# Kernel tuning notes

Hardware: AMD Instinct MI355X
Metric: run time of the kernel (lower is better)

Reference implementation:

```python
import jax, jax.numpy as jnp
import numpy as np

D_MODEL = 1024
N_HEADS = 16
D_HEAD = D_MODEL // N_HEADS


def setup_inputs() -> dict:
    key = jax.random.key(0)
    ks = jax.random.split(key, 5)
    scale = 1.0 / np.sqrt(D_MODEL)
    x = jax.random.normal(ks[0], (4, 2048, D_MODEL), dtype=jnp.float32)
    w_qkv = jax.random.normal(ks[1], (D_MODEL, 3 * D_MODEL), dtype=jnp.float32) * scale
    b_qkv = jax.random.normal(ks[2], (3 * D_MODEL,), dtype=jnp.float32) * 0.02
    w_out = jax.random.normal(ks[3], (D_MODEL, D_MODEL), dtype=jnp.float32) * scale
    b_out = jax.random.normal(ks[4], (D_MODEL,), dtype=jnp.float32) * 0.02
    return {"x": x, "w_qkv": w_qkv, "b_qkv": b_qkv, "w_out": w_out, "b_out": b_out}


def reference(x, w_qkv, b_qkv, w_out, b_out):
    b, s, _ = x.shape
    qkv = jnp.einsum("bsd,de->bse", x, w_qkv) + b_qkv  # [b, s, 3*d_model]
    q, k, v = jnp.split(qkv, 3, axis=-1)
    # [b, s, d_model] -> [b, h, s, d_head]
    def heads(t):
        return t.reshape(b, s, N_HEADS, D_HEAD).transpose(0, 2, 1, 3)
    q, k, v = heads(q), heads(k), heads(v)
    scale = 1.0 / np.sqrt(D_HEAD).astype(np.float32)
    attn = jnp.einsum("bhqd,bhkd->bhqk", q, k) * scale  # [b, h, s, s]
    attn = jax.nn.softmax(attn, axis=-1)
    out = jnp.einsum("bhqk,bhkd->bhqd", attn, v)  # [b, h, s, d_head]
    out = out.transpose(0, 2, 1, 3).reshape(b, s, D_MODEL)
    return jnp.einsum("bsd,de->bse", out, w_out) + b_out
```

## Files before the change

### kernel.cpp

```cpp
#include <hip/hip_runtime.h>
#include <hip/hip_bf16.h>

typedef unsigned short u16;
typedef unsigned int u32;
typedef __attribute__((ext_vector_type(8))) short bf16x8;
typedef __attribute__((ext_vector_type(4))) float f32x4;
typedef __attribute__((ext_vector_type(16))) float f32x16;

#define MFMA16(a, b, c) __builtin_amdgcn_mfma_f32_16x16x32_bf16((a), (b), (c), 0, 0, 0)
#define MFMA32(a, b, c) __builtin_amdgcn_mfma_f32_32x32x16_bf16((a), (b), (c), 0, 0, 0)

__device__ __forceinline__ u16 f2bf(float f) {
    u32 u;
    __builtin_memcpy(&u, &f, 4);
    u32 r = (u + 0x7FFFu + ((u >> 16) & 1u)) >> 16;
    return (u16)r;
}

__device__ __forceinline__ u32 pk_bf16(float a, float b) {
    u32 r;
    asm("v_cvt_pk_bf16_f32 %0, %1, %2" : "=v"(r) : "v"(a), "v"(b));
    return r;
}

__device__ __forceinline__ void gload16(const void* g, void* l) {
    __builtin_amdgcn_global_load_lds((const __attribute__((address_space(1))) u32*)g,
                                     (__attribute__((address_space(3))) u32*)l, 16, 0, 0);
}

__global__ __launch_bounds__(256) void cvt_bf16(const float* __restrict__ in, u16* __restrict__ out) {
    size_t i = ((size_t)blockIdx.x * 256 + threadIdx.x) * 8;
    f32x4 a = *(const f32x4*)(in + i);
    f32x4 b = *(const f32x4*)(in + i + 4);
    union {
        bf16x8 v;
        u16 s[8];
    } r;
    r.s[0] = f2bf(a[0]);
    r.s[1] = f2bf(a[1]);
    r.s[2] = f2bf(a[2]);
    r.s[3] = f2bf(a[3]);
    r.s[4] = f2bf(b[0]);
    r.s[5] = f2bf(b[1]);
    r.s[6] = f2bf(b[2]);
    r.s[7] = f2bf(b[3]);
    *(bf16x8*)(out + i) = r.v;
}

__global__ __launch_bounds__(256) void transpose_f32_bf16(const float* __restrict__ in,
                                                          u16* __restrict__ out, int R, int C) {
    __shared__ u16 t[64][65];
    const int c0 = blockIdx.x * 64, r0 = blockIdx.y * 64;
    const int tid = threadIdx.x;
#pragma unroll
    for (int i = 0; i < 16; ++i) {
        int idx = i * 256 + tid;
        int r = idx >> 6, c = idx & 63;
        t[r][c] = f2bf(in[(size_t)(r0 + r) * C + c0 + c]);
    }
    __syncthreads();
#pragma unroll
    for (int i = 0; i < 16; ++i) {
        int idx = i * 256 + tid;
        int cc = idx >> 6, rr = idx & 63;
        out[(size_t)(c0 + cc) * R + r0 + rr] = t[rr][cc];
    }
}

template <int ROWS>
__device__ __forceinline__ void stage_tile(const u16* gbase, int stride_e, u16* lds, int tid) {
    const int wbase16 = (tid & ~63) * 8;
#pragma unroll
    for (int i = 0; i < ROWS / 32; ++i) {
        int chunk = i * 256 + tid;
        int r = chunk >> 3;
        int c = chunk & 7;
        int sc = c ^ (r & 7);
        const u16* src = gbase + (size_t)r * stride_e + sc * 8;
        u16* dst = lds + i * 2048 + wbase16;
        gload16(src, dst);
    }
}

#define QSCALE 0.1803368801111243f

__global__ __launch_bounds__(256) void gemm_bt(const u16* __restrict__ A, const u16* __restrict__ Bt,
                                               const float* __restrict__ bias, u16* __restrict__ Cb,
                                               u16* __restrict__ vt, float* __restrict__ Cf, int M,
                                               int N, int K, int Cstride, int split) {
    __shared__ __align__(16) u16 As[128 * 64];
    __shared__ __align__(16) u16 Bs[128 * 64];
    const int tid = threadIdx.x;
    const int lane = tid & 63, wid = tid >> 6;
    const int wr = wid >> 1, wc = wid & 1;
    const int g = lane >> 4, l15 = lane & 15;
    const int m0 = blockIdx.y * 128, n0 = blockIdx.x * 128;

    f32x4 acc[4][4] = {};

    for (int k0 = 0; k0 < K; k0 += 64) {
        __syncthreads();
        stage_tile<128>(A + (size_t)m0 * K + k0, K, As, tid);
        stage_tile<128>(Bt + (size_t)n0 * K + k0, K, Bs, tid);
        __syncthreads();
        bf16x8 af[4][2], bf[4][2];
#pragma unroll
        for (int m = 0; m < 4; ++m) {
            int row = wr * 64 + m * 16 + l15;
#pragma unroll
            for (int t = 0; t < 2; ++t) {
                int off = row * 128 + (((t * 4 + g) ^ (row & 7)) * 16);
                af[m][t] = *(const bf16x8*)((const char*)As + off);
            }
        }
#pragma unroll
        for (int n = 0; n < 4; ++n) {
            int row = wc * 64 + n * 16 + l15;
#pragma unroll
            for (int t = 0; t < 2; ++t) {
                int off = row * 128 + (((t * 4 + g) ^ (row & 7)) * 16);
                bf[n][t] = *(const bf16x8*)((const char*)Bs + off);
            }
        }
#pragma unroll
        for (int m = 0; m < 4; ++m)
#pragma unroll
            for (int n = 0; n < 4; ++n) {
                acc[m][n] = MFMA16(af[m][0], bf[n][0], acc[m][n]);
                acc[m][n] = MFMA16(af[m][1], bf[n][1], acc[m][n]);
            }
    }

#pragma unroll
    for (int m = 0; m < 4; ++m) {
        int row0 = m0 + wr * 64 + m * 16 + g * 4;
#pragma unroll
        for (int n = 0; n < 4; ++n) {
            int col = n0 + wc * 64 + n * 16 + l15;
            float bs = bias ? bias[col] : 0.0f;
            if (!split) {
#pragma unroll
                for (int rr = 0; rr < 4; ++rr)
                    Cf[(size_t)(row0 + rr) * Cstride + col] = acc[m][n][rr] + bs;
            } else {
                if (col < 2048) {
                    float scale = (col < 1024) ? QSCALE : 1.0f;
#pragma unroll
                    for (int rr = 0; rr < 4; ++rr)
                        Cb[(size_t)(row0 + rr) * 2048 + col] = f2bf((acc[m][n][rr] + bs) * scale);
                } else {
                    int e2 = col - 2048;
                    int h = e2 >> 6, dh = e2 & 63;
                    int b = row0 >> 11, s = row0 & 2047;
                    u32 lo = pk_bf16(acc[m][n][0] + bs, acc[m][n][1] + bs);
                    u32 hi = pk_bf16(acc[m][n][2] + bs, acc[m][n][3] + bs);
                    u32* dst = (u32*)&vt[((size_t)((b * 16 + h) * 64 + dh)) * 2048 + s];
                    dst[0] = lo;
                    dst[1] = hi;
                }
            }
        }
    }
}

__global__ __launch_bounds__(256, 4) void attn_fwd(const u16* __restrict__ qk,
                                                   const u16* __restrict__ vt,
                                                   u16* __restrict__ out) {
    __shared__ __align__(16) u16 Ks[2][64 * 64];
    __shared__ __align__(16) u16 Vs[2][64 * 64];
    const int tid = threadIdx.x;
    const int lane = tid & 63, w = tid >> 6;
    const int hi = lane >> 5, l31 = lane & 31;
    const int bh = blockIdx.y, b = bh >> 4, h = bh & 15;
    const int q0w = blockIdx.x * 128 + w * 32;
    const size_t qrowbase = (size_t)b * 2048 + q0w;

    bf16x8 qf[4];
#pragma unroll
    for (int c = 0; c < 4; ++c)
        qf[c] = *(const bf16x8*)&qk[(qrowbase + l31) * 2048 + h * 64 + c * 16 + hi * 8];

    float l_r = 0.f;
    f32x16 acc[2] = {};
    const f32x16 FZERO = {};

    const u16* kbase = qk + (size_t)b * 2048 * 2048 + 1024 + h * 64;
    const u16* vbase = vt + (size_t)bh * 64 * 2048;

    const int wb16 = (tid & ~63) * 8;
    const int ch0 = tid, ch1 = 256 + tid;
    const int r0c = ch0 >> 3, s0c = (ch0 & 7) ^ (r0c & 7);
    const int r1c = ch1 >> 3, s1c = (ch1 & 7) ^ (r1c & 7);
    const u16* kp0 = kbase + r0c * 2048 + s0c * 8;
    const u16* kp1 = kbase + r1c * 2048 + s1c * 8;
    const u16* vp0 = vbase + r0c * 2048 + s0c * 8;
    const u16* vp1 = vbase + r1c * 2048 + s1c * 8;
    const int KADV = 64 * 2048;

    const int swz8 = l31 & 7;
    const int rowB = l31 * 128;
    int exorH[4];
#pragma unroll
    for (int c = 0; c < 4; ++c) exorH[c] = ((2 * c + hi) ^ swz8) * 16;
    int exorV[2][2];
#pragma unroll
    for (int kb = 0; kb < 2; ++kb)
#pragma unroll
        for (int t = 0; t < 2; ++t) exorV[kb][t] = ((4 * kb + 2 * t + hi) ^ swz8) * 16;

    {
        u16* kd = &Ks[0][0] + wb16;
        u16* vd = &Vs[0][0] + wb16;
        gload16(kp0, kd);
        gload16(kp1, kd + 2048);
        gload16(vp0, vd);
        gload16(vp1, vd + 2048);
        kp0 += KADV;
        kp1 += KADV;
        vp0 += 64;
        vp1 += 64;
    }
    __syncthreads();

    int cur = 0;
    for (int kv0 = 0; kv0 < 2048; kv0 += 64) {
        if (kv0 + 64 < 2048) {
            u16* kd = &Ks[cur ^ 1][0] + wb16;
            u16* vd = &Vs[cur ^ 1][0] + wb16;
            gload16(kp0, kd);
            gload16(kp1, kd + 2048);
            gload16(vp0, vd);
            gload16(vp1, vd + 2048);
            kp0 += KADV;
            kp1 += KADV;
            vp0 += 64;
            vp1 += 64;
        }
        const char* ksr = (const char*)&Ks[cur][0] + rowB;
        const char* vsr = (const char*)&Vs[cur][0] + rowB;

        f32x16 sA, sB;
        {
            bf16x8 ka0 = *(const bf16x8*)(ksr + exorH[0]);
            bf16x8 kb0 = *(const bf16x8*)(ksr + exorH[0] + 4096);
            sA = MFMA32(ka0, qf[0], FZERO);
            sB = MFMA32(kb0, qf[0], FZERO);
#pragma unroll
            for (int c = 1; c < 4; ++c) {
                bf16x8 ka = *(const bf16x8*)(ksr + exorH[c]);
                bf16x8 kb = *(const bf16x8*)(ksr + exorH[c] + 4096);
                sA = MFMA32(ka, qf[c], sA);
                sB = MFMA32(kb, qf[c], sB);
            }
        }

#pragma unroll
        for (int kb = 0; kb < 2; ++kb) {
            const f32x16& s = kb ? sB : sA;
            float rs0 = 0.f, rs1 = 0.f;
            u32 pk[8];
#pragma unroll
            for (int j = 0; j < 8; ++j) {
                float p0 = __builtin_amdgcn_exp2f(s[2 * j]);
                float p1 = __builtin_amdgcn_exp2f(s[2 * j + 1]);
                rs0 += p0;
                rs1 += p1;
                pk[j] = pk_bf16(p0, p1);
            }
            l_r += rs0 + rs1;

            auto s02 = __builtin_amdgcn_permlane32_swap(pk[0], pk[2], false, false);
            auto s13 = __builtin_amdgcn_permlane32_swap(pk[1], pk[3], false, false);
            auto s46 = __builtin_amdgcn_permlane32_swap(pk[4], pk[6], false, false);
            auto s57 = __builtin_amdgcn_permlane32_swap(pk[5], pk[7], false, false);
            union {
                bf16x8 v;
                u32 u[4];
            } f0, f1;
            f0.u[0] = s02[0];
            f0.u[1] = s13[0];
            f0.u[2] = s02[1];
            f0.u[3] = s13[1];
            f1.u[0] = s46[0];
            f1.u[1] = s57[0];
            f1.u[2] = s46[1];
            f1.u[3] = s57[1];

#pragma unroll
            for (int d = 0; d < 2; ++d) {
                bf16x8 v0 = *(const bf16x8*)(vsr + exorV[kb][0] + d * 4096);
                bf16x8 v1 = *(const bf16x8*)(vsr + exorV[kb][1] + d * 4096);
                acc[d] = MFMA32(f0.v, v0, acc[d]);
                acc[d] = MFMA32(f1.v, v1, acc[d]);
            }
        }
        __syncthreads();
        cur ^= 1;
    }

    float l_tot = l_r + __shfl_xor(l_r, 32);
    float lr[16];
#pragma unroll
    for (int r = 0; r < 16; ++r) lr[r] = __shfl(l_tot, (r & 3) + 8 * (r >> 2) + 4 * hi);
#pragma unroll
    for (int d = 0; d < 2; ++d)
#pragma unroll
        for (int r = 0; r < 16; ++r) {
            int q = (r & 3) + 8 * (r >> 2) + 4 * hi;
            out[(qrowbase + q) * 1024 + h * 64 + d * 32 + l31] = f2bf(acc[d][r] / lr[r]);
        }
}

extern "C" void kernel_launch(void* const* d_in, const int* in_sizes, int n_in, void* d_out,
                              int out_size, void* d_ws, size_t ws_size, hipStream_t stream) {
    const float* x = (const float*)d_in[0];
    const float* w_qkv = (const float*)d_in[1];
    const float* b_qkv = (const float*)d_in[2];
    const float* w_out = (const float*)d_in[3];
    const float* b_out = (const float*)d_in[4];
    float* out = (float*)d_out;

    u16* ws = (u16*)d_ws;
    u16* xbf = ws;
    u16* WqkvT = xbf + (size_t)8192 * 1024;
    u16* WoutT = WqkvT + (size_t)3072 * 1024;
    u16* qkbuf = WoutT + (size_t)1024 * 1024;
    u16* vtbuf = qkbuf + (size_t)8192 * 2048;
    u16* attnb = vtbuf + (size_t)64 * 64 * 2048;

    cvt_bf16<<<4096, 256, 0, stream>>>(x, xbf);
    transpose_f32_bf16<<<dim3(48, 16), 256, 0, stream>>>(w_qkv, WqkvT, 1024, 3072);
    transpose_f32_bf16<<<dim3(16, 16), 256, 0, stream>>>(w_out, WoutT, 1024, 1024);

    gemm_bt<<<dim3(24, 64), 256, 0, stream>>>(xbf, WqkvT, b_qkv, qkbuf, vtbuf, nullptr, 8192, 3072,
                                              1024, 2048, 1);

    attn_fwd<<<dim3(16, 64), 256, 0, stream>>>(qkbuf, vtbuf, attnb);

    gemm_bt<<<dim3(8, 64), 256, 0, stream>>>(attnb, WoutT, b_out, nullptr, nullptr, out, 8192, 1024,
                                             1024, 1024, 0);
}
```

Measured before the change: 210.1 us.

## Process two 32-row query tiles per wave to reuse K/V fragments

Each wave now handles 64 query rows, split into two 32-row sub-tiles that share the K and V fragments loaded from LDS. The block covers 256 queries, so the grid halves and launch bounds drop to 2 blocks per SM to allow the extra registers. This cuts LDS reads and global K/V staging per query. MFMA sections are also wrapped in s_setprio to favour matrix issue. The cost is higher register pressure, lower occupancy and fewer blocks (512) to spread across the CUs.

New measurement: 196.0 us. -6.7%, faster.

```diff
diff --git a/kernel.cpp b/kernel.cpp
--- a/kernel.cpp
+++ b/kernel.cpp
@@ -163,7 +163,7 @@
     }
 }
 
-__global__ __launch_bounds__(256, 4) void attn_fwd(const u16* __restrict__ qk,
+__global__ __launch_bounds__(256, 2) void attn_fwd(const u16* __restrict__ qk,
                                                    const u16* __restrict__ vt,
                                                    u16* __restrict__ out) {
     __shared__ __align__(16) u16 Ks[2][64 * 64];
@@ -172,16 +172,18 @@
     const int lane = tid & 63, w = tid >> 6;
     const int hi = lane >> 5, l31 = lane & 31;
     const int bh = blockIdx.y, b = bh >> 4, h = bh & 15;
-    const int q0w = blockIdx.x * 128 + w * 32;
+    const int q0w = blockIdx.x * 256 + w * 64;
     const size_t qrowbase = (size_t)b * 2048 + q0w;
 
-    bf16x8 qf[4];
-#pragma unroll
-    for (int c = 0; c < 4; ++c)
-        qf[c] = *(const bf16x8*)&qk[(qrowbase + l31) * 2048 + h * 64 + c * 16 + hi * 8];
-
-    float l_r = 0.f;
-    f32x16 acc[2] = {};
+    bf16x8 qfA[4], qfB[4];
+#pragma unroll
+    for (int c = 0; c < 4; ++c) {
+        qfA[c] = *(const bf16x8*)&qk[(qrowbase + l31) * 2048 + h * 64 + c * 16 + hi * 8];
+        qfB[c] = *(const bf16x8*)&qk[(qrowbase + 32 + l31) * 2048 + h * 64 + c * 16 + hi * 8];
+    }
+
+    float l_rA = 0.f, l_rB = 0.f;
+    f32x16 accA[2] = {}, accB[2] = {};
     const f32x16 FZERO = {};
 
     const u16* kbase = qk + (size_t)b * 2048 * 2048 + 1024 + h * 64;
@@ -239,76 +241,89 @@
         const char* ksr = (const char*)&Ks[cur][0] + rowB;
         const char* vsr = (const char*)&Vs[cur][0] + rowB;
 
-        f32x16 sA, sB;
-        {
-            bf16x8 ka0 = *(const bf16x8*)(ksr + exorH[0]);
-            bf16x8 kb0 = *(const bf16x8*)(ksr + exorH[0] + 4096);
-            sA = MFMA32(ka0, qf[0], FZERO);
-            sB = MFMA32(kb0, qf[0], FZERO);
-#pragma unroll
-            for (int c = 1; c < 4; ++c) {
-                bf16x8 ka = *(const bf16x8*)(ksr + exorH[c]);
-                bf16x8 kb = *(const bf16x8*)(ksr + exorH[c] + 4096);
-                sA = MFMA32(ka, qf[c], sA);
-                sB = MFMA32(kb, qf[c], sB);
-            }
-        }
-
 #pragma unroll
         for (int kb = 0; kb < 2; ++kb) {
-            const f32x16& s = kb ? sB : sA;
-            float rs0 = 0.f, rs1 = 0.f;
-            u32 pk[8];
-#pragma unroll
-            for (int j = 0; j < 8; ++j) {
-                float p0 = __builtin_amdgcn_exp2f(s[2 * j]);
-                float p1 = __builtin_amdgcn_exp2f(s[2 * j + 1]);
-                rs0 += p0;
-                rs1 += p1;
-                pk[j] = pk_bf16(p0, p1);
-            }
-            l_r += rs0 + rs1;
-
-            auto s02 = __builtin_amdgcn_permlane32_swap(pk[0], pk[2], false, false);
-            auto s13 = __builtin_amdgcn_permlane32_swap(pk[1], pk[3], false, false);
-            auto s46 = __builtin_amdgcn_permlane32_swap(pk[4], pk[6], false, false);
-            auto s57 = __builtin_amdgcn_permlane32_swap(pk[5], pk[7], false, false);
-            union {
-                bf16x8 v;
-                u32 u[4];
-            } f0, f1;
-            f0.u[0] = s02[0];
-            f0.u[1] = s13[0];
-            f0.u[2] = s02[1];
-            f0.u[3] = s13[1];
-            f1.u[0] = s46[0];
-            f1.u[1] = s57[0];
-            f1.u[2] = s46[1];
-            f1.u[3] = s57[1];
-
-#pragma unroll
-            for (int d = 0; d < 2; ++d) {
-                bf16x8 v0 = *(const bf16x8*)(vsr + exorV[kb][0] + d * 4096);
-                bf16x8 v1 = *(const bf16x8*)(vsr + exorV[kb][1] + d * 4096);
-                acc[d] = MFMA32(f0.v, v0, acc[d]);
-                acc[d] = MFMA32(f1.v, v1, acc[d]);
+            bf16x8 kf0 = *(const bf16x8*)(ksr + exorH[0] + kb * 4096);
+            bf16x8 kf1 = *(const bf16x8*)(ksr + exorH[1] + kb * 4096);
+            bf16x8 kf2 = *(const bf16x8*)(ksr + exorH[2] + kb * 4096);
+            bf16x8 kf3 = *(const bf16x8*)(ksr + exorH[3] + kb * 4096);
+            bf16x8 v00 = *(const bf16x8*)(vsr + exorV[kb][0]);
+            bf16x8 v01 = *(const bf16x8*)(vsr + exorV[kb][1]);
+            bf16x8 v10 = *(const bf16x8*)(vsr + exorV[kb][0] + 4096);
+            bf16x8 v11 = *(const bf16x8*)(vsr + exorV[kb][1] + 4096);
+
+#pragma unroll
+            for (int qb = 0; qb < 2; ++qb) {
+                const bf16x8* qf = qb ? qfB : qfA;
+                f32x16* acc = qb ? accB : accA;
+
+                __builtin_amdgcn_s_setprio(1);
+                f32x16 s = MFMA32(kf0, qf[0], FZERO);
+                s = MFMA32(kf1, qf[1], s);
+                s = MFMA32(kf2, qf[2], s);
+                s = MFMA32(kf3, qf[3], s);
+                __builtin_amdgcn_s_setprio(0);
+
+                float rs0 = 0.f, rs1 = 0.f;
+                u32 pk[8];
+#pragma unroll
+                for (int j = 0; j < 8; ++j) {
+                    float p0 = __builtin_amdgcn_exp2f(s[2 * j]);
+                    float p1 = __builtin_amdgcn_exp2f(s[2 * j + 1]);
+                    rs0 += p0;
+                    rs1 += p1;
+                    pk[j] = pk_bf16(p0, p1);
+                }
+                if (qb)
+                    l_rB += rs0 + rs1;
+                else
+                    l_rA += rs0 + rs1;
+
+                auto s02 = __builtin_amdgcn_permlane32_swap(pk[0], pk[2], false, false);
+                auto s13 = __builtin_amdgcn_permlane32_swap(pk[1], pk[3], false, false);
+                auto s46 = __builtin_amdgcn_permlane32_swap(pk[4], pk[6], false, false);
+                auto s57 = __builtin_amdgcn_permlane32_swap(pk[5], pk[7], false, false);
+                union {
+                    bf16x8 v;
+                    u32 u[4];
+                } f0, f1;
+                f0.u[0] = s02[0];
+                f0.u[1] = s13[0];
+                f0.u[2] = s02[1];
+                f0.u[3] = s13[1];
+                f1.u[0] = s46[0];
+                f1.u[1] = s57[0];
+                f1.u[2] = s46[1];
+                f1.u[3] = s57[1];
+
+                __builtin_amdgcn_s_setprio(1);
+                acc[0] = MFMA32(f0.v, v00, acc[0]);
+                acc[0] = MFMA32(f1.v, v01, acc[0]);
+                acc[1] = MFMA32(f0.v, v10, acc[1]);
+                acc[1] = MFMA32(f1.v, v11, acc[1]);
+                __builtin_amdgcn_s_setprio(0);
             }
         }
         __syncthreads();
         cur ^= 1;
     }
 
-    float l_tot = l_r + __shfl_xor(l_r, 32);
-    float lr[16];
-#pragma unroll
-    for (int r = 0; r < 16; ++r) lr[r] = __shfl(l_tot, (r & 3) + 8 * (r >> 2) + 4 * hi);
-#pragma unroll
-    for (int d = 0; d < 2; ++d)
-#pragma unroll
-        for (int r = 0; r < 16; ++r) {
-            int q = (r & 3) + 8 * (r >> 2) + 4 * hi;
-            out[(qrowbase + q) * 1024 + h * 64 + d * 32 + l31] = f2bf(acc[d][r] / lr[r]);
-        }
+#pragma unroll
+    for (int qb = 0; qb < 2; ++qb) {
+        float l_r = qb ? l_rB : l_rA;
+        const f32x16* acc = qb ? accB : accA;
+        float l_tot = l_r + __shfl_xor(l_r, 32);
+        float lr[16];
+#pragma unroll
+        for (int r = 0; r < 16; ++r) lr[r] = __shfl(l_tot, (r & 3) + 8 * (r >> 2) + 4 * hi);
+#pragma unroll
+        for (int d = 0; d < 2; ++d)
+#pragma unroll
+            for (int r = 0; r < 16; ++r) {
+                int q = qb * 32 + (r & 3) + 8 * (r >> 2) + 4 * hi;
+                out[(qrowbase + q) * 1024 + h * 64 + d * 32 + l31] = f2bf(acc[d][r] / lr[r]);
+            }
+    }
 }
 
 extern "C" void kernel_launch(void* const* d_in, const int* in_sizes, int n_in, void* d_out,
@@ -335,7 +350,7 @@
     gemm_bt<<<dim3(24, 64), 256, 0, stream>>>(xbf, WqkvT, b_qkv, qkbuf, vtbuf, nullptr, 8192, 3072,
                                               1024, 2048, 1);
 
-    attn_fwd<<<dim3(16, 64), 256, 0, stream>>>(qkbuf, vtbuf, attnb);
+    attn_fwd<<<dim3(8, 64), 256, 0, stream>>>(qkbuf, vtbuf, attnb);
 
     gemm_bt<<<dim3(8, 64), 256, 0, stream>>>(attnb, WoutT, b_out, nullptr, nullptr, out, 8192, 1024,
                                              1024, 1024, 0);
```
